# Optimization experiments

Measured on AMD Instinct MI355X. Metric: run time of the kernel, lower is better.

Reference implementation:

```python
import jax, jax.numpy as jnp
import numpy as np

D_MODEL = 1024
N_HEADS = 16
D_K = D_MODEL // N_HEADS


def setup_inputs() -> dict:
    key = jax.random.key(0)
    ks = jax.random.split(key, 11)
    B, S = 2, 2048
    scale = 0.02
    inp = {
        "q": jax.random.normal(ks[0], (B, S, D_MODEL), jnp.float32),
        "k": jax.random.normal(ks[1], (B, S, D_MODEL), jnp.float32),
        "v": jax.random.normal(ks[2], (B, S, D_MODEL), jnp.float32),
        "w_q": jax.random.normal(ks[3], (D_MODEL, D_MODEL), jnp.float32) * scale,
        "b_q": jnp.zeros((D_MODEL,), jnp.float32),
        "w_k": jax.random.normal(ks[4], (D_MODEL, D_MODEL), jnp.float32) * scale,
        "b_k": jnp.zeros((D_MODEL,), jnp.float32),
        "w_v": jax.random.normal(ks[5], (D_MODEL, D_MODEL), jnp.float32) * scale,
        "b_v": jnp.zeros((D_MODEL,), jnp.float32),
        "w_o": jax.random.normal(ks[6], (D_MODEL, D_MODEL), jnp.float32) * scale,
        "b_o": jnp.zeros((D_MODEL,), jnp.float32),
    }
    return inp


def reference(q, k, v, w_q, b_q, w_k, b_k, w_v, b_v, w_o, b_o):
    B, S, _ = q.shape
    # projections (torch Linear: x @ W.T + b); split into heads -> [B, H, S, d]
    def proj(x, w, b):
        return (x @ w.T + b).reshape(B, S, N_HEADS, D_K).transpose(0, 2, 1, 3)
    qh = proj(q, w_q, b_q)
    kh = proj(k, w_k, b_k)
    vh = proj(v, w_v, b_v)
    scores = jnp.einsum("bhqd,bhkd->bhqk", qh, kh) / jnp.sqrt(
        jnp.asarray(D_K, jnp.float32))
    attn = jax.nn.softmax(scores, axis=-1)  # dropout = identity (eval)
    out = jnp.einsum("bhqk,bhkd->bhqd", attn, vh)
    out = out.transpose(0, 2, 1, 3).reshape(B, S, D_MODEL)
    return out @ w_o.T + b_o
```

## Files before the change

kernel.cpp:

```cpp
#include <hip/hip_runtime.h>

typedef unsigned short u16;
typedef unsigned int u32;
typedef __attribute__((ext_vector_type(4))) unsigned short u16x4;
typedef __attribute__((ext_vector_type(8))) unsigned short u16x8;
typedef __attribute__((ext_vector_type(8))) __bf16 bf16x8;
typedef __attribute__((ext_vector_type(4))) float f32x4;
typedef __attribute__((ext_vector_type(16))) float f32x16;

#define SEQ 2048
#define DMODEL 1024
#define LDP 3072
#define MM (DMODEL * DMODEL)
#define SC 0.18033688f

__device__ __forceinline__ u16 f2bf(float f) {
  unsigned u = __builtin_bit_cast(unsigned, f);
  u = (u + 0x7fffu + ((u >> 16) & 1u)) >> 16;
  return (u16)u;
}

__device__ __forceinline__ u32 cvtpk(float lo, float hi) {
  u32 r;
  asm volatile("v_cvt_pk_bf16_f32 %0, %1, %2" : "=v"(r) : "v"(lo), "v"(hi));
  return r;
}

__device__ __forceinline__ float fexp2(float x) {
#if __has_builtin(__builtin_amdgcn_exp2f)
  return __builtin_amdgcn_exp2f(x);
#else
  return exp2f(x);
#endif
}

__device__ __forceinline__ bf16x8 ldbf8(const u16* p) {
  return __builtin_bit_cast(bf16x8, *(const u16x8*)p);
}
__device__ __forceinline__ bf16x8 ldbf8c(const char* p) {
  return __builtin_bit_cast(bf16x8, *(const u16x8*)p);
}

__device__ __forceinline__ f32x4 mfma16(bf16x8 a, bf16x8 b, f32x4 c) {
  return __builtin_amdgcn_mfma_f32_16x16x32_bf16(a, b, c, 0, 0, 0);
}
__device__ __forceinline__ f32x16 mfma32(bf16x8 a, bf16x8 b, f32x16 c) {
  return __builtin_amdgcn_mfma_f32_32x32x16_bf16(a, b, c, 0, 0, 0);
}

__device__ __forceinline__ void gl16(const void* g, void* l) {
  __builtin_amdgcn_global_load_lds(
      (__attribute__((address_space(1))) void*)(size_t)g,
      (__attribute__((address_space(3))) void*)l, 16, 0, 0);
}

__global__ void cast_all_k(const float* __restrict__ q, const float* __restrict__ k,
                           const float* __restrict__ v, const float* __restrict__ wq,
                           const float* __restrict__ wk, const float* __restrict__ wv,
                           const float* __restrict__ wo, u16* __restrict__ dq,
                           u16* __restrict__ dk, u16* __restrict__ dv,
                           u16* __restrict__ wqkv, u16* __restrict__ wob) {
  int b = blockIdx.x;
  const float* s;
  u16* d;
  if (b < 6144) {
    const int z = b >> 11;
    s = z == 0 ? q : z == 1 ? k : v;
    d = z == 0 ? dq : z == 1 ? dk : dv;
    b &= 2047;
  } else {
    const int z = (b - 6144) >> 9;
    s = z == 0 ? wq : z == 1 ? wk : z == 2 ? wv : wo;
    d = z < 3 ? wqkv + (size_t)z * MM : wob;
    b = (b - 6144) & 511;
  }
  const size_t i = ((size_t)b * blockDim.x + threadIdx.x) * 8;
  const float4 a = *(const float4*)(s + i);
  const float4 c = *(const float4*)(s + i + 4);
  u16x8 o;
  o[0] = f2bf(a.x); o[1] = f2bf(a.y); o[2] = f2bf(a.z); o[3] = f2bf(a.w);
  o[4] = f2bf(c.x); o[5] = f2bf(c.y); o[6] = f2bf(c.z); o[7] = f2bf(c.w);
  *(u16x8*)(d + i) = o;
}

template <int OMODE>
__device__ __forceinline__ void gemm_bt_body(const u16* __restrict__ A,
                                             const u16* __restrict__ Bw,
                                             const float* __restrict__ bias,
                                             void* __restrict__ Cv, const int K,
                                             const int ldc, const int ncol0,
                                             const int m0, const int n0,
                                             const float osc) {
  __shared__ u16 As[128 * 32];
  __shared__ u16 Bs[128 * 32];
  const int tid = threadIdx.x;
  const int lane = tid & 63;
  const int w = tid >> 6;
  const int l15 = lane & 15;
  const int lg = lane >> 4;

  f32x4 acc[4][4] = {};

  const int arow = (w >> 1) * 64 + l15;
  const int brow = (w & 1) * 64 + l15;
  const int kfb = lg * 16;

  const int strow = w * 32 + (lane >> 2);
  const u16* Ag = A + (size_t)(m0 + strow) * K + (lane & 3) * 8;
  const u16* Bg = Bw + (size_t)(n0 + strow) * K + (lane & 3) * 8;
  const size_t rstep = (size_t)16 * K;
  char* AsL0 = (char*)As + w * 32 * 64;
  char* AsL1 = AsL0 + 16 * 64;
  char* BsL0 = (char*)Bs + w * 32 * 64;
  char* BsL1 = BsL0 + 16 * 64;

  for (int k0 = 0; k0 < K; k0 += 32) {
    __syncthreads();
    gl16(Ag + k0, AsL0);
    gl16(Ag + k0 + rstep, AsL1);
    gl16(Bg + k0, BsL0);
    gl16(Bg + k0 + rstep, BsL1);
    __syncthreads();
    bf16x8 af[4], bfv[4];
#pragma unroll
    for (int t = 0; t < 4; ++t) {
      af[t] = ldbf8c((char*)As + (arow + t * 16) * 64 + kfb);
      bfv[t] = ldbf8c((char*)Bs + (brow + t * 16) * 64 + kfb);
    }
    __builtin_amdgcn_s_setprio(1);
#pragma unroll
    for (int i = 0; i < 4; ++i)
#pragma unroll
      for (int j = 0; j < 4; ++j) acc[i][j] = mfma16(af[i], bfv[j], acc[i][j]);
    __builtin_amdgcn_s_setprio(0);
  }

  const int mrow = (w >> 1) * 64 + lg * 4;
  const int ncol = (w & 1) * 64 + l15;
#pragma unroll
  for (int j = 0; j < 4; ++j) {
    const int gn = n0 + ncol + j * 16;
    const float bia = bias[gn];
#pragma unroll
    for (int i = 0; i < 4; ++i) {
      const int gmb = m0 + mrow + i * 16;
#pragma unroll
      for (int r = 0; r < 4; ++r) {
        const float val = (acc[i][j][r] + bia) * osc;
        const int gm = gmb + r;
        if (OMODE == 0) {
          ((float*)Cv)[(size_t)gm * ldc + gn] = val;
        } else if (OMODE == 1) {
          ((u16*)Cv)[(size_t)gm * ldc + ncol0 + gn] = f2bf(val);
        } else {
          const int bb = gm >> 11, ss = gm & 2047;
          const int ssp = (ss & ~12) | ((ss & 4) << 1) | ((ss & 8) >> 1);
          const int hh = gn >> 6, dd = gn & 63;
          ((u16*)Cv)[(((size_t)(bb * 16 + hh) * 64 + dd) << 11) + ssp] = f2bf(val);
        }
      }
    }
  }
}

__global__ __launch_bounds__(256, 3) void gemm_qkv_k(
    const u16* __restrict__ qb, const u16* __restrict__ kb,
    const u16* __restrict__ vb, const u16* __restrict__ wqkv,
    const float* __restrict__ bq, const float* __restrict__ bk,
    const float* __restrict__ bv, u16* __restrict__ proj, u16* __restrict__ vtb) {
  const int b = blockIdx.x;
  const int xcd = b & 7;
  const int i = b >> 3;
  const int z = i >> 5;
  const int j = i & 31;
  const int m0 = (xcd * 4 + (j >> 3)) * 128;
  const int n0 = (j & 7) * 128;
  if (z == 2)
    gemm_bt_body<2>(vb, wqkv + 2 * (size_t)MM, bv, vtb, DMODEL, 0, 0, m0, n0,
                    1.0f);
  else
    gemm_bt_body<1>(z == 0 ? qb : kb, wqkv + (size_t)z * MM, z == 0 ? bq : bk,
                    proj, DMODEL, LDP, z * DMODEL, m0, n0, z == 0 ? SC : 1.0f);
}

__global__ __launch_bounds__(256, 3) void gemm_o_k(const u16* __restrict__ attnb,
                                                   const u16* __restrict__ wob,
                                                   const float* __restrict__ bo,
                                                   float* __restrict__ out) {
  const int b = blockIdx.x;
  const int xcd = b & 7;
  const int i = b >> 3;
  const int m0 = (xcd * 4 + (i >> 3)) * 128;
  const int n0 = (i & 7) * 128;
  gemm_bt_body<0>(attnb, wob, bo, out, DMODEL, DMODEL, 0, m0, n0, 1.0f);
}

__global__ __launch_bounds__(512, 2) void attn_k(const u16* __restrict__ proj,
                                                 const u16* __restrict__ vtb,
                                                 u16* __restrict__ outa) {
  __shared__ __align__(16) char smem[65536];
  const int b = blockIdx.x;
  const int slot = b >> 3;
  const int bh = (b & 7) * 4 + (slot >> 3);
  const int qB = (slot & 7) * 256;
  const int tid = threadIdx.x;
  const int lane = tid & 63;
  const int w = tid >> 6;
  const int g = w >> 2;
  const int wg = w & 3;
  const size_t rb = (size_t)(bh >> 4) * SEQ;
  const int h = bh & 15;
  const int l31 = lane & 31;
  const int hi = lane >> 5;
  const int swzk = (l31 & 7) << 4;

  char* const gbase = smem + g * 32768;

  const int qW = qB + wg * 64;
  const u16* qpA = proj + (rb + qW + l31) * LDP + h * 64 + hi * 8;
  const u16* qpB = qpA + (size_t)32 * LDP;
  bf16x8 qfA[4], qfB[4];
#pragma unroll
  for (int km = 0; km < 4; ++km) {
    qfA[km] = ldbf8(qpA + km * 16);
    qfB[km] = ldbf8(qpB + km * 16);
  }

  const int cxe = ((lane & 7) ^ (lane >> 3)) * 8;
  const int row0 = wg * 16 + (lane >> 3);
  const int row1 = row0 + 8;
  const u16* kg = proj + rb * LDP + DMODEL + h * 64;
  const u16* vg = vtb + (size_t)bh * 64 * SEQ;
  const int kvbase = g * (SEQ / 2);
  const u16* ks0 = kg + (size_t)(kvbase + row0) * LDP + cxe;
  const u16* ks1 = kg + (size_t)(kvbase + row1) * LDP + cxe;
  const u16* vs0 = vg + (size_t)row0 * SEQ + kvbase + cxe;
  const u16* vs1 = vg + (size_t)row1 * SEQ + kvbase + cxe;

#define STAGE(P, KOFF)                                                   \
  {                                                                      \
    char* kb_ = gbase + (P) * 8192;                                      \
    char* vb_ = gbase + 16384 + (P) * 8192;                              \
    gl16(ks0 + (size_t)(KOFF) * LDP, kb_ + (wg * 2 + 0) * 1024);         \
    gl16(ks1 + (size_t)(KOFF) * LDP, kb_ + (wg * 2 + 1) * 1024);         \
    gl16(vs0 + (KOFF), vb_ + (wg * 2 + 0) * 1024);                       \
    gl16(vs1 + (KOFF), vb_ + (wg * 2 + 1) * 1024);                       \
  }

  f32x16 oaA0 = {}, oaA1 = {}, oaB0 = {}, oaB1 = {};
  float lrunA = 0.f, lrunB = 0.f;
  int p = 0;

  STAGE(0, 0);
  __syncthreads();

  for (int it = 0; it < SEQ / 128; ++it) {
    if (it + 1 < SEQ / 128) STAGE(p ^ 1, (it + 1) * 64);
    const char* kp = gbase + p * 8192;
    const char* vp = gbase + 16384 + p * 8192;
    f32x16 sA0 = {}, sA1 = {}, sB0 = {}, sB1 = {};
    __builtin_amdgcn_s_setprio(1);
#pragma unroll
    for (int km = 0; km < 4; ++km) {
      const int co = (km * 32 + hi * 16) ^ swzk;
      const bf16x8 k0 = ldbf8c(kp + l31 * 128 + co);
      const bf16x8 k1 = ldbf8c(kp + (32 + l31) * 128 + co);
      sA0 = mfma32(k0, qfA[km], sA0);
      sB0 = mfma32(k0, qfB[km], sB0);
      sA1 = mfma32(k1, qfA[km], sA1);
      sB1 = mfma32(k1, qfB[km], sB1);
    }
    __builtin_amdgcn_s_setprio(0);

#pragma unroll
    for (int r = 0; r < 16; ++r) sA0[r] = fexp2(sA0[r]);
#pragma unroll
    for (int r = 0; r < 16; ++r) sA1[r] = fexp2(sA1[r]);
#pragma unroll
    for (int r = 0; r < 16; ++r) sB0[r] = fexp2(sB0[r]);
#pragma unroll
    for (int r = 0; r < 16; ++r) sB1[r] = fexp2(sB1[r]);
#define SUM16(V)                                                        \
    ((((V[0] + V[1]) + (V[2] + V[3])) + ((V[4] + V[5]) + (V[6] + V[7]))) + \
     (((V[8] + V[9]) + (V[10] + V[11])) + ((V[12] + V[13]) + (V[14] + V[15]))))
    float rsA = SUM16(sA0) + SUM16(sA1);
    float rsB = SUM16(sB0) + SUM16(sB1);
#undef SUM16
    rsA += __shfl_xor(rsA, 32);
    rsB += __shfl_xor(rsB, 32);
    lrunA += rsA;
    lrunB += rsB;

    __builtin_amdgcn_s_setprio(1);
#define PCHUNK2(SA, SB, G, M)                                            \
    {                                                                    \
      u16x8 pbuA, pbuB;                                                  \
      ((u32*)&pbuA)[0] = cvtpk(SA[G + 0], SA[G + 1]);                    \
      ((u32*)&pbuA)[1] = cvtpk(SA[G + 2], SA[G + 3]);                    \
      ((u32*)&pbuA)[2] = cvtpk(SA[G + 4], SA[G + 5]);                    \
      ((u32*)&pbuA)[3] = cvtpk(SA[G + 6], SA[G + 7]);                    \
      ((u32*)&pbuB)[0] = cvtpk(SB[G + 0], SB[G + 1]);                    \
      ((u32*)&pbuB)[1] = cvtpk(SB[G + 2], SB[G + 3]);                    \
      ((u32*)&pbuB)[2] = cvtpk(SB[G + 4], SB[G + 5]);                    \
      ((u32*)&pbuB)[3] = cvtpk(SB[G + 6], SB[G + 7]);                    \
      const bf16x8 pbA = __builtin_bit_cast(bf16x8, pbuA);               \
      const bf16x8 pbB = __builtin_bit_cast(bf16x8, pbuB);               \
      const int vc = ((M) * 32 + hi * 16) ^ swzk;                        \
      const bf16x8 v0 = ldbf8c(vp + l31 * 128 + vc);                     \
      const bf16x8 v1 = ldbf8c(vp + (32 + l31) * 128 + vc);              \
      oaA0 = mfma32(v0, pbA, oaA0);                                      \
      oaB0 = mfma32(v0, pbB, oaB0);                                      \
      oaA1 = mfma32(v1, pbA, oaA1);                                      \
      oaB1 = mfma32(v1, pbB, oaB1);                                      \
    }
    PCHUNK2(sA0, sB0, 0, 0)
    PCHUNK2(sA0, sB0, 8, 1)
    PCHUNK2(sA1, sB1, 0, 2)
    PCHUNK2(sA1, sB1, 8, 3)
#undef PCHUNK2
    __builtin_amdgcn_s_setprio(0);
    __syncthreads();
    p ^= 1;
  }
#undef STAGE

  float* sc = (float*)smem;
  const int col = wg * 64 + lane;
  if (g == 1) {
#pragma unroll
    for (int r = 0; r < 16; ++r) sc[r * 256 + col] = oaA0[r];
#pragma unroll
    for (int r = 0; r < 16; ++r) sc[(16 + r) * 256 + col] = oaA1[r];
    sc[32 * 256 + col] = lrunA;
  }
  __syncthreads();
  if (g == 0) {
#pragma unroll
    for (int r = 0; r < 16; ++r) oaA0[r] += sc[r * 256 + col];
#pragma unroll
    for (int r = 0; r < 16; ++r) oaA1[r] += sc[(16 + r) * 256 + col];
    lrunA += sc[32 * 256 + col];
  }
  __syncthreads();
  if (g == 1) {
#pragma unroll
    for (int r = 0; r < 16; ++r) sc[r * 256 + col] = oaB0[r];
#pragma unroll
    for (int r = 0; r < 16; ++r) sc[(16 + r) * 256 + col] = oaB1[r];
    sc[32 * 256 + col] = lrunB;
  }
  __syncthreads();
  if (g == 0) {
#pragma unroll
    for (int r = 0; r < 16; ++r) oaB0[r] += sc[r * 256 + col];
#pragma unroll
    for (int r = 0; r < 16; ++r) oaB1[r] += sc[(16 + r) * 256 + col];
    lrunB += sc[32 * 256 + col];

    const float invA = 1.0f / lrunA;
    u16* orowA = outa + (rb + qW + l31) * DMODEL + h * 64 + hi * 4;
#pragma unroll
    for (int gg = 0; gg < 4; ++gg) {
      u16x4 st0, st1;
      ((u32*)&st0)[0] = cvtpk(oaA0[4 * gg + 0] * invA, oaA0[4 * gg + 1] * invA);
      ((u32*)&st0)[1] = cvtpk(oaA0[4 * gg + 2] * invA, oaA0[4 * gg + 3] * invA);
      *(u16x4*)(orowA + 8 * gg) = st0;
      ((u32*)&st1)[0] = cvtpk(oaA1[4 * gg + 0] * invA, oaA1[4 * gg + 1] * invA);
      ((u32*)&st1)[1] = cvtpk(oaA1[4 * gg + 2] * invA, oaA1[4 * gg + 3] * invA);
      *(u16x4*)(orowA + 32 + 8 * gg) = st1;
    }
    const float invB = 1.0f / lrunB;
    u16* orowB = orowA + (size_t)32 * DMODEL;
#pragma unroll
    for (int gg = 0; gg < 4; ++gg) {
      u16x4 st0, st1;
      ((u32*)&st0)[0] = cvtpk(oaB0[4 * gg + 0] * invB, oaB0[4 * gg + 1] * invB);
      ((u32*)&st0)[1] = cvtpk(oaB0[4 * gg + 2] * invB, oaB0[4 * gg + 3] * invB);
      *(u16x4*)(orowB + 8 * gg) = st0;
      ((u32*)&st1)[0] = cvtpk(oaB1[4 * gg + 0] * invB, oaB1[4 * gg + 1] * invB);
      ((u32*)&st1)[1] = cvtpk(oaB1[4 * gg + 2] * invB, oaB1[4 * gg + 3] * invB);
      *(u16x4*)(orowB + 32 + 8 * gg) = st1;
    }
  }
}

extern "C" void kernel_launch(void* const* d_in, const int* in_sizes, int n_in,
                              void* d_out, int out_size, void* d_ws, size_t ws_size,
                              hipStream_t stream) {
  const float* q  = (const float*)d_in[0];
  const float* k  = (const float*)d_in[1];
  const float* v  = (const float*)d_in[2];
  const float* wq = (const float*)d_in[3];
  const float* bq = (const float*)d_in[4];
  const float* wk = (const float*)d_in[5];
  const float* bk = (const float*)d_in[6];
  const float* wv = (const float*)d_in[7];
  const float* bv = (const float*)d_in[8];
  const float* wo = (const float*)d_in[9];
  const float* bo = (const float*)d_in[10];

  const size_t NTOK = (size_t)2 * SEQ;
  const size_t NELE = NTOK * DMODEL;
  u16* qb    = (u16*)d_ws;
  u16* kb    = qb + NELE;
  u16* vb    = kb + NELE;
  u16* wqkv  = vb + NELE;
  u16* wob   = wqkv + 3 * (size_t)MM;
  u16* projb = wob + (size_t)MM;
  u16* vtb   = projb + NTOK * LDP;
  u16* attnb = qb;

  cast_all_k<<<8192, 256, 0, stream>>>(q, k, v, wq, wk, wv, wo, qb, kb, vb,
                                       wqkv, wob);
  gemm_qkv_k<<<768, 256, 0, stream>>>(qb, kb, vb, wqkv, bq, bk, bv, projb, vtb);
  attn_k<<<256, 512, 0, stream>>>(projb, vtb, attnb);
  gemm_o_k<<<256, 256, 0, stream>>>(attnb, wob, bo, (float*)d_out);
}
```

Measured before the change: 120.2 us.

## Double GEMM K-tile to 64 with XOR-swizzled LDS layout

The projection GEMM body now stages 64-wide K tiles instead of 32, which halves the number of barrier pairs per K loop and issues more global-to-LDS loads per sync. The LDS layout becomes 128-byte rows, and an XOR swizzle applied to the global source column is matched by the same swizzle on the fragment reads to avoid bank conflicts. LDS use doubles and the swizzle adds index arithmetic. The load-compute pattern is still unpipelined within each tile.

```diff
diff --git a/kernel.cpp b/kernel.cpp
--- a/kernel.cpp
+++ b/kernel.cpp
@@ -91,8 +91,8 @@
                                              const int ldc, const int ncol0,
                                              const int m0, const int n0,
                                              const float osc) {
-  __shared__ u16 As[128 * 32];
-  __shared__ u16 Bs[128 * 32];
+  __shared__ u16 As[128 * 64];
+  __shared__ u16 Bs[128 * 64];
   const int tid = threadIdx.x;
   const int lane = tid & 63;
   const int w = tid >> 6;
@@ -103,36 +103,43 @@
 
   const int arow = (w >> 1) * 64 + l15;
   const int brow = (w & 1) * 64 + l15;
-  const int kfb = lg * 16;
-
-  const int strow = w * 32 + (lane >> 2);
-  const u16* Ag = A + (size_t)(m0 + strow) * K + (lane & 3) * 8;
-  const u16* Bg = Bw + (size_t)(n0 + strow) * K + (lane & 3) * 8;
-  const size_t rstep = (size_t)16 * K;
-  char* AsL0 = (char*)As + w * 32 * 64;
-  char* AsL1 = AsL0 + 16 * 64;
-  char* BsL0 = (char*)Bs + w * 32 * 64;
-  char* BsL1 = BsL0 + 16 * 64;
-
-  for (int k0 = 0; k0 < K; k0 += 32) {
+  const int swz = (l15 & 7) << 4;
+
+  const u16* Ags[4];
+  const u16* Bgs[4];
+#pragma unroll
+  for (int j = 0; j < 4; ++j) {
+    const int c = w * 64 + lane + j * 256;
+    const int row = c >> 3;
+    const int sc = ((c & 7) ^ (row & 7)) * 8;
+    Ags[j] = A + (size_t)(m0 + row) * K + sc;
+    Bgs[j] = Bw + (size_t)(n0 + row) * K + sc;
+  }
+
+  for (int k0 = 0; k0 < K; k0 += 64) {
     __syncthreads();
-    gl16(Ag + k0, AsL0);
-    gl16(Ag + k0 + rstep, AsL1);
-    gl16(Bg + k0, BsL0);
-    gl16(Bg + k0 + rstep, BsL1);
+#pragma unroll
+    for (int j = 0; j < 4; ++j) {
+      gl16(Ags[j] + k0, (char*)As + (w + j * 4) * 1024);
+      gl16(Bgs[j] + k0, (char*)Bs + (w + j * 4) * 1024);
+    }
     __syncthreads();
-    bf16x8 af[4], bfv[4];
-#pragma unroll
-    for (int t = 0; t < 4; ++t) {
-      af[t] = ldbf8c((char*)As + (arow + t * 16) * 64 + kfb);
-      bfv[t] = ldbf8c((char*)Bs + (brow + t * 16) * 64 + kfb);
-    }
-    __builtin_amdgcn_s_setprio(1);
-#pragma unroll
-    for (int i = 0; i < 4; ++i)
-#pragma unroll
-      for (int j = 0; j < 4; ++j) acc[i][j] = mfma16(af[i], bfv[j], acc[i][j]);
-    __builtin_amdgcn_s_setprio(0);
+#pragma unroll
+    for (int kk = 0; kk < 2; ++kk) {
+      const int cb = (kk * 64 + lg * 16) ^ swz;
+      bf16x8 af[4], bfv[4];
+#pragma unroll
+      for (int t = 0; t < 4; ++t) {
+        af[t] = ldbf8c((char*)As + (arow + t * 16) * 128 + cb);
+        bfv[t] = ldbf8c((char*)Bs + (brow + t * 16) * 128 + cb);
+      }
+      __builtin_amdgcn_s_setprio(1);
+#pragma unroll
+      for (int i = 0; i < 4; ++i)
+#pragma unroll
+        for (int j = 0; j < 4; ++j) acc[i][j] = mfma16(af[i], bfv[j], acc[i][j]);
+      __builtin_amdgcn_s_setprio(0);
+    }
   }
 
   const int mrow = (w >> 1) * 64 + lg * 4;
```

New measurement: 126.9 us. 1.06x slower.
